# Kernel tuning notes

Measured on AMD Instinct MI355X. Metric: run time of the kernel, lower is better.

## Reference

```python
import jax, jax.numpy as jnp
import numpy as np
from jax import lax

LN_EPS = 1e-5          # F.layer_norm default eps
W_EPS = 1e-7           # eps in ste_weights
Q_EPS = 1e-5           # BitLinear.eps used in activation clamp
Q_RANGE = 128          # 2**(num_bits-1), num_bits=8
DIM_IN = 2048
DIM_OUT = 8192
N_TOKENS = 8192


def setup_inputs() -> dict:
    key = jax.random.key(0)
    k1, k2 = jax.random.split(key)
    x = jax.random.normal(k1, (N_TOKENS, DIM_IN), dtype=jnp.float32)
    # nn.Linear default init: U(-1/sqrt(fan_in), 1/sqrt(fan_in))
    bound = 1.0 / np.sqrt(DIM_IN)
    weight = jax.random.uniform(k2, (DIM_OUT, DIM_IN), dtype=jnp.float32,
                                minval=-bound, maxval=bound)
    return {"x": x, "weight": weight}


def _bitlinear(x, weight):
    # layer_norm over feature dim, no affine params
    mu = jnp.mean(x, axis=-1, keepdims=True)
    var = jnp.mean(jnp.square(x - mu), axis=-1, keepdims=True)
    normed = (x - mu) * lax.rsqrt(var + LN_EPS)

    # scalars come from .item() in torch -> detached constants
    input_gamma = lax.stop_gradient(jnp.max(jnp.abs(normed)))
    w_gamma = lax.stop_gradient(jnp.mean(jnp.abs(weight)))

    # ternarize weights with straight-through estimator
    w_bin_ng = jnp.clip(jnp.round(weight / (w_gamma + W_EPS)), -1.0, 1.0)
    w_bin = weight + lax.stop_gradient(w_bin_ng - weight)

    # quantize activations to int8 range (kept in float, as in the source)
    q_in = jnp.clip(normed * (Q_RANGE / input_gamma),
                    -Q_RANGE + Q_EPS, Q_RANGE - Q_EPS)

    out = q_in @ w_bin.T  # [N, dim_out]; bias=False since mult_bias=False
    return out * (input_gamma * w_gamma / Q_RANGE)


def reference(x, weight):
    proj = _bitlinear(x, weight)               # [N, DIM_OUT]
    h, gate = jnp.split(proj, 2, axis=-1)      # chunk(2, dim=-1)
    return h * jax.nn.silu(gate)               # mult_bias == 1.0
```

## Files before the change

kernel.cpp:

```cpp
#include <hip/hip_runtime.h>
#include <hip/hip_bf16.h>
#include <cstdint>


#define N_TOK   8192
#define DIMIN   2048
#define DIMOUT  8192
#define NOUT    4096
#define W_ELEMS 16777216.0f
#define NPART   1024

typedef _Float16 f16x8 __attribute__((ext_vector_type(8)));
typedef _Float16 f16x4 __attribute__((ext_vector_type(4)));
typedef float    f32x4 __attribute__((ext_vector_type(4)));

__global__ __launch_bounds__(256) void ln_wsum_k(
    const float* __restrict__ x, const float* __restrict__ w,
    _Float16* __restrict__ qA, float* __restrict__ wpart) {
    const int b = blockIdx.x;
    const int t = threadIdx.x;
    if (b < N_TOK) {
        __shared__ float sh[8];
        const float4* xr = (const float4*)(x + (size_t)b * DIMIN);
        float4 a = xr[2 * t];
        float4 c = xr[2 * t + 1];
        float s = (a.x + a.y) + (a.z + a.w) + ((c.x + c.y) + (c.z + c.w));
#pragma unroll
        for (int o = 32; o > 0; o >>= 1) s += __shfl_down(s, o, 64);
        if ((t & 63) == 0) sh[t >> 6] = s;
        __syncthreads();
        const float mu = (sh[0] + sh[1] + sh[2] + sh[3]) * (1.0f / DIMIN);

        float d0 = a.x - mu, d1 = a.y - mu, d2 = a.z - mu, d3 = a.w - mu;
        float d4 = c.x - mu, d5 = c.y - mu, d6 = c.z - mu, d7 = c.w - mu;
        float ss = d0*d0 + d1*d1 + d2*d2 + d3*d3 + d4*d4 + d5*d5 + d6*d6 + d7*d7;
#pragma unroll
        for (int o = 32; o > 0; o >>= 1) ss += __shfl_down(ss, o, 64);
        if ((t & 63) == 0) sh[4 + (t >> 6)] = ss;
        __syncthreads();
        const float var = (sh[4] + sh[5] + sh[6] + sh[7]) * (1.0f / DIMIN);
        const float r = rsqrtf(var + 1e-5f);
        f16x8 o;
        o[0] = (_Float16)(d0 * r); o[1] = (_Float16)(d1 * r);
        o[2] = (_Float16)(d2 * r); o[3] = (_Float16)(d3 * r);
        o[4] = (_Float16)(d4 * r); o[5] = (_Float16)(d5 * r);
        o[6] = (_Float16)(d6 * r); o[7] = (_Float16)(d7 * r);
        ((f16x8*)(qA + (size_t)b * DIMIN))[t] = o;
    } else {
        const int p = b - N_TOK;
        float acc = 0.0f;
        const float4* w4 = (const float4*)w;
        for (unsigned i = (unsigned)p * 256u + t; i < 4194304u; i += 262144u) {
            float4 v = w4[i];
            acc += (fabsf(v.x) + fabsf(v.y)) + (fabsf(v.z) + fabsf(v.w));
        }
        __shared__ float shw[4];
#pragma unroll
        for (int o = 32; o > 0; o >>= 1) acc += __shfl_down(acc, o, 64);
        if ((t & 63) == 0) shw[t >> 6] = acc;
        __syncthreads();
        if (t == 0) wpart[p] = (shw[0] + shw[1]) + (shw[2] + shw[3]);
    }
}

__global__ __launch_bounds__(256) void ternW_k(
    const float* __restrict__ w, const float* __restrict__ wpart,
    float* __restrict__ sc, _Float16* __restrict__ q) {
    const int t = threadIdx.x;
    __shared__ float sh[4];
    float4 p = ((const float4*)wpart)[t];
    float acc = (p.x + p.y) + (p.z + p.w);
#pragma unroll
    for (int o = 32; o > 0; o >>= 1) acc += __shfl_down(acc, o, 64);
    if ((t & 63) == 0) sh[t >> 6] = acc;
    __syncthreads();
    const float wg = ((sh[0] + sh[1]) + (sh[2] + sh[3])) * (1.0f / W_ELEMS);
    if (blockIdx.x == 0 && t == 0) sc[0] = wg;
    const float invw = 1.0f / (wg + 1e-7f);
    for (unsigned i = blockIdx.x * 256u + t; i < 4194304u; i += 262144u) {
        float4 v = ((const float4*)w)[i];
        f16x4 o;
        o.x = (_Float16)fminf(fmaxf(rintf(v.x * invw), -1.0f), 1.0f);
        o.y = (_Float16)fminf(fmaxf(rintf(v.y * invw), -1.0f), 1.0f);
        o.z = (_Float16)fminf(fmaxf(rintf(v.z * invw), -1.0f), 1.0f);
        o.w = (_Float16)fminf(fmaxf(rintf(v.w * invw), -1.0f), 1.0f);
        ((f16x4*)q)[i] = o;
    }
}

__device__ __forceinline__ void ld16(const _Float16* g, _Float16* l) {
    __builtin_amdgcn_global_load_lds(
        (const __attribute__((address_space(1))) unsigned int*)g,
        (__attribute__((address_space(3))) unsigned int*)l, 16, 0, 0);
}

#define STAGE(par) do {                                              \
    _Float16* dA_ = sm + ((par) << 14) + (wave << 9);                \
    _Float16* dB_ = sm + 32768 + ((par) << 14) + (wave << 9);        \
    ld16(pa,            dA_);                                        \
    ld16(pa + 131072,   dA_ + 4096);                                 \
    ld16(pa + 262144,   dA_ + 8192);                                 \
    ld16(pa + 393216,   dA_ + 12288);                                \
    ld16(pb,            dB_);                                        \
    ld16(pb + 131072,   dB_ + 4096);                                 \
    ld16(pb + 8388608,  dB_ + 8192);                                 \
    ld16(pb + 8519680,  dB_ + 12288);                                \
    pa += 64; pb += 64;                                              \
} while (0)

__global__ __launch_bounds__(512, 2) void gemm_glu_k(
    const _Float16* __restrict__ Aq, const _Float16* __restrict__ Wq,
    const float* __restrict__ sc, float* __restrict__ out) {

    __shared__ __align__(16) _Float16 sm[65536];

    const int tid  = threadIdx.x;
    const int wave = tid >> 6;
    const int lane = tid & 63;

    const int swz = ((blockIdx.x & 7) << 7) + (blockIdx.x >> 3);
    const int m0 = (swz >> 5) << 8;
    const int n0 = (swz & 31) << 7;

    const int rs = (wave << 3) + (lane >> 3);
    const int kc = (((lane & 7) ^ ((lane >> 3) & 7)) << 3);
    const _Float16* pa = Aq + (size_t)(m0 + rs) * DIMIN + kc;
    const _Float16* pb = Wq + (size_t)(n0 + rs) * DIMIN + kc;

    const int fr   = lane & 15;
    const int quad = lane >> 4;
    const int xr   = fr & 7;
    const int wm = (wave >> 1) << 6;
    const int wn = (wave & 1) << 6;
    const int a0off = (wm + fr) * 64 + ((quad ^ xr) << 3);
    const int a1off = (wm + fr) * 64 + (((quad + 4) ^ xr) << 3);
    const int b0off = (wn + fr) * 64 + ((quad ^ xr) << 3);
    const int b1off = (wn + fr) * 64 + (((quad + 4) ^ xr) << 3);

    const float s = sc[0];

    f32x4 z = {0.0f, 0.0f, 0.0f, 0.0f};
    f32x4 acc_h[4][4], acc_g[4][4];
#pragma unroll
    for (int i = 0; i < 4; ++i)
#pragma unroll
        for (int j = 0; j < 4; ++j) { acc_h[i][j] = z; acc_g[i][j] = z; }

    STAGE(0);
    asm volatile("s_waitcnt vmcnt(2)" ::: "memory");
    __builtin_amdgcn_s_barrier();

    f16x8 a[4], b[4];
#pragma unroll 2
    for (int t = 0; t < 32; ++t) {
        const _Float16* Ac = sm + ((t & 1) << 14);
        const _Float16* Bc = sm + 32768 + ((t & 1) << 14);
        const bool more = (t < 31);

#pragma unroll
        for (int i = 0; i < 4; ++i) {
            a[i] = *(const f16x8*)(Ac + a0off + (i << 10));
            b[i] = *(const f16x8*)(Bc + b0off + (i << 10));
        }
        if (more) STAGE((t + 1) & 1);
        __builtin_amdgcn_s_barrier();
        asm volatile("s_waitcnt lgkmcnt(0)" ::: "memory");
        __builtin_amdgcn_s_setprio(1);
#pragma unroll
        for (int mi = 0; mi < 4; ++mi)
#pragma unroll
            for (int ni = 0; ni < 4; ++ni)
                acc_h[mi][ni] = __builtin_amdgcn_mfma_f32_16x16x32_f16(
                    a[mi], b[ni], acc_h[mi][ni], 0, 0, 0);
        __builtin_amdgcn_s_setprio(0);
        if (more) asm volatile("s_waitcnt vmcnt(8)" ::: "memory");
        else      asm volatile("s_waitcnt vmcnt(0)" ::: "memory");
        __builtin_amdgcn_s_barrier();

#pragma unroll
        for (int i = 0; i < 4; ++i)
            b[i] = *(const f16x8*)(Bc + 8192 + b0off + (i << 10));
        __builtin_amdgcn_s_barrier();
        asm volatile("s_waitcnt lgkmcnt(0)" ::: "memory");
        __builtin_amdgcn_s_setprio(1);
#pragma unroll
        for (int mi = 0; mi < 4; ++mi)
#pragma unroll
            for (int ni = 0; ni < 4; ++ni)
                acc_g[mi][ni] = __builtin_amdgcn_mfma_f32_16x16x32_f16(
                    a[mi], b[ni], acc_g[mi][ni], 0, 0, 0);
        __builtin_amdgcn_s_setprio(0);
        __builtin_amdgcn_s_barrier();

#pragma unroll
        for (int i = 0; i < 4; ++i) {
            a[i] = *(const f16x8*)(Ac + a1off + (i << 10));
            b[i] = *(const f16x8*)(Bc + b1off + (i << 10));
        }
        __builtin_amdgcn_s_barrier();
        asm volatile("s_waitcnt lgkmcnt(0)" ::: "memory");
        __builtin_amdgcn_s_setprio(1);
#pragma unroll
        for (int mi = 0; mi < 4; ++mi)
#pragma unroll
            for (int ni = 0; ni < 4; ++ni)
                acc_h[mi][ni] = __builtin_amdgcn_mfma_f32_16x16x32_f16(
                    a[mi], b[ni], acc_h[mi][ni], 0, 0, 0);
        __builtin_amdgcn_s_setprio(0);
        __builtin_amdgcn_s_barrier();

#pragma unroll
        for (int i = 0; i < 4; ++i)
            b[i] = *(const f16x8*)(Bc + 8192 + b1off + (i << 10));
        __builtin_amdgcn_s_barrier();
        asm volatile("s_waitcnt lgkmcnt(0)" ::: "memory");
        __builtin_amdgcn_s_setprio(1);
#pragma unroll
        for (int mi = 0; mi < 4; ++mi)
#pragma unroll
            for (int ni = 0; ni < 4; ++ni)
                acc_g[mi][ni] = __builtin_amdgcn_mfma_f32_16x16x32_f16(
                    a[mi], b[ni], acc_g[mi][ni], 0, 0, 0);
        __builtin_amdgcn_s_setprio(0);
        if (more) asm volatile("s_waitcnt vmcnt(2)" ::: "memory");
        __builtin_amdgcn_s_barrier();
    }

    const int er = quad << 2;
#pragma unroll
    for (int mi = 0; mi < 4; ++mi)
#pragma unroll
        for (int ni = 0; ni < 4; ++ni)
#pragma unroll
            for (int r = 0; r < 4; ++r) {
                const int m = m0 + wm + (mi << 4) + er + r;
                const int n = n0 + wn + (ni << 4) + fr;
                const float h = acc_h[mi][ni][r] * s;
                const float g = acc_g[mi][ni][r] * s;
                out[(size_t)m * NOUT + n] = h * g / (1.0f + __expf(-g));
            }
}

extern "C" void kernel_launch(void* const* d_in, const int* in_sizes, int n_in,
                              void* d_out, int out_size, void* d_ws, size_t ws_size,
                              hipStream_t stream) {
    const float* x = (const float*)d_in[0];
    const float* w = (const float*)d_in[1];
    float* out = (float*)d_out;

    char* ws = (char*)d_ws;
    float* sc    = (float*)ws;
    float* wpart = (float*)(ws + 4096);
    _Float16* qA = (_Float16*)(ws + 16384);
    _Float16* wB = (_Float16*)(ws + 16384 + 33554432);

    ln_wsum_k<<<N_TOK + NPART, 256, 0, stream>>>(x, w, qA, wpart);
    ternW_k<<<NPART, 256, 0, stream>>>(w, wpart, sc, wB);

    gemm_glu_k<<<dim3(1024), dim3(512), 0, stream>>>(qA, wB, sc, out);
}
```

Before: 471.3 us.

## Interleave next-tile global-to-LDS loads across MFMA phases and peel last iteration

Instead of issuing all eight global-to-LDS loads for the next K tile at the start of each iteration, the loads are split into pairs spread across the four MFMA phases. The final iteration is peeled so the loop body has no 'more' conditionals. The intent is to smooth memory issue pressure and overlap loads with compute more evenly. The cost is tighter vmcnt accounting, since a missed wait could read stale LDS data, and the loop is no longer unrolled by two.

Result: faster. 450.5 us (-4.4%).

```diff
diff --git a/kernel.cpp b/kernel.cpp
--- a/kernel.cpp
+++ b/kernel.cpp
@@ -94,19 +94,28 @@
         (__attribute__((address_space(3))) unsigned int*)l, 16, 0, 0);
 }
 
-#define STAGE(par) do {                                              \
-    _Float16* dA_ = sm + ((par) << 14) + (wave << 9);                \
-    _Float16* dB_ = sm + 32768 + ((par) << 14) + (wave << 9);        \
-    ld16(pa,            dA_);                                        \
-    ld16(pa + 131072,   dA_ + 4096);                                 \
-    ld16(pa + 262144,   dA_ + 8192);                                 \
-    ld16(pa + 393216,   dA_ + 12288);                                \
-    ld16(pb,            dB_);                                        \
-    ld16(pb + 131072,   dB_ + 4096);                                 \
-    ld16(pb + 8388608,  dB_ + 8192);                                 \
-    ld16(pb + 8519680,  dB_ + 12288);                                \
-    pa += 64; pb += 64;                                              \
-} while (0)
+
+#define BAR    __builtin_amdgcn_s_barrier()
+#define LGKM0  asm volatile("s_waitcnt lgkmcnt(0)" ::: "memory")
+#define VMC(n) asm volatile("s_waitcnt vmcnt(" #n ")" ::: "memory")
+#define PRIO1  __builtin_amdgcn_s_setprio(1)
+#define PRIO0  __builtin_amdgcn_s_setprio(0)
+
+#define MFMA16(ACC)                                                       \
+    _Pragma("unroll") for (int mi = 0; mi < 4; ++mi)                      \
+    _Pragma("unroll") for (int ni = 0; ni < 4; ++ni)                      \
+        ACC[mi][ni] = __builtin_amdgcn_mfma_f32_16x16x32_f16(             \
+            a[mi], b[ni], ACC[mi][ni], 0, 0, 0);
+
+#define DS_AB(AOFF, BOFF_)                                                \
+    _Pragma("unroll") for (int i = 0; i < 4; ++i) {                       \
+        a[i] = *(const f16x8*)(Ac + (AOFF) + (i << 10));                  \
+        b[i] = *(const f16x8*)(Bc + (BOFF_) + (i << 10));                 \
+    }
+
+#define DS_B(BOFF_)                                                       \
+    _Pragma("unroll") for (int i = 0; i < 4; ++i)                         \
+        b[i] = *(const f16x8*)(Bc + (BOFF_) + (i << 10));
 
 __global__ __launch_bounds__(512, 2) void gemm_glu_k(
     const _Float16* __restrict__ Aq, const _Float16* __restrict__ Wq,
@@ -146,84 +155,85 @@
 #pragma unroll
         for (int j = 0; j < 4; ++j) { acc_h[i][j] = z; acc_g[i][j] = z; }
 
-    STAGE(0);
-    asm volatile("s_waitcnt vmcnt(2)" ::: "memory");
-    __builtin_amdgcn_s_barrier();
+    {
+        _Float16* dA = sm + (wave << 9);
+        _Float16* dB = dA + 32768;
+        ld16(pb,           dB);
+        ld16(pb + 131072,  dB + 4096);
+        ld16(pa,           dA);
+        ld16(pa + 131072,  dA + 4096);
+        ld16(pa + 262144,  dA + 8192);
+        ld16(pa + 393216,  dA + 12288);
+        ld16(pb + 8388608, dB + 8192);
+        ld16(pb + 8519680, dB + 12288);
+        pa += 64; pb += 64;
+    }
+    VMC(2);
+    BAR;
 
     f16x8 a[4], b[4];
-#pragma unroll 2
-    for (int t = 0; t < 32; ++t) {
+    for (int t = 0; t < 31; ++t) {
         const _Float16* Ac = sm + ((t & 1) << 14);
-        const _Float16* Bc = sm + 32768 + ((t & 1) << 14);
-        const bool more = (t < 31);
-
-#pragma unroll
-        for (int i = 0; i < 4; ++i) {
-            a[i] = *(const f16x8*)(Ac + a0off + (i << 10));
-            b[i] = *(const f16x8*)(Bc + b0off + (i << 10));
-        }
-        if (more) STAGE((t + 1) & 1);
-        __builtin_amdgcn_s_barrier();
-        asm volatile("s_waitcnt lgkmcnt(0)" ::: "memory");
-        __builtin_amdgcn_s_setprio(1);
-#pragma unroll
-        for (int mi = 0; mi < 4; ++mi)
-#pragma unroll
-            for (int ni = 0; ni < 4; ++ni)
-                acc_h[mi][ni] = __builtin_amdgcn_mfma_f32_16x16x32_f16(
-                    a[mi], b[ni], acc_h[mi][ni], 0, 0, 0);
-        __builtin_amdgcn_s_setprio(0);
-        if (more) asm volatile("s_waitcnt vmcnt(8)" ::: "memory");
-        else      asm volatile("s_waitcnt vmcnt(0)" ::: "memory");
-        __builtin_amdgcn_s_barrier();
-
-#pragma unroll
-        for (int i = 0; i < 4; ++i)
-            b[i] = *(const f16x8*)(Bc + 8192 + b0off + (i << 10));
-        __builtin_amdgcn_s_barrier();
-        asm volatile("s_waitcnt lgkmcnt(0)" ::: "memory");
-        __builtin_amdgcn_s_setprio(1);
-#pragma unroll
-        for (int mi = 0; mi < 4; ++mi)
-#pragma unroll
-            for (int ni = 0; ni < 4; ++ni)
-                acc_g[mi][ni] = __builtin_amdgcn_mfma_f32_16x16x32_f16(
-                    a[mi], b[ni], acc_g[mi][ni], 0, 0, 0);
-        __builtin_amdgcn_s_setprio(0);
-        __builtin_amdgcn_s_barrier();
-
-#pragma unroll
-        for (int i = 0; i < 4; ++i) {
-            a[i] = *(const f16x8*)(Ac + a1off + (i << 10));
-            b[i] = *(const f16x8*)(Bc + b1off + (i << 10));
-        }
-        __builtin_amdgcn_s_barrier();
-        asm volatile("s_waitcnt lgkmcnt(0)" ::: "memory");
-        __builtin_amdgcn_s_setprio(1);
-#pragma unroll
-        for (int mi = 0; mi < 4; ++mi)
-#pragma unroll
-            for (int ni = 0; ni < 4; ++ni)
-                acc_h[mi][ni] = __builtin_amdgcn_mfma_f32_16x16x32_f16(
-                    a[mi], b[ni], acc_h[mi][ni], 0, 0, 0);
-        __builtin_amdgcn_s_setprio(0);
-        __builtin_amdgcn_s_barrier();
-
-#pragma unroll
-        for (int i = 0; i < 4; ++i)
-            b[i] = *(const f16x8*)(Bc + 8192 + b1off + (i << 10));
-        __builtin_amdgcn_s_barrier();
-        asm volatile("s_waitcnt lgkmcnt(0)" ::: "memory");
-        __builtin_amdgcn_s_setprio(1);
-#pragma unroll
-        for (int mi = 0; mi < 4; ++mi)
-#pragma unroll
-            for (int ni = 0; ni < 4; ++ni)
-                acc_g[mi][ni] = __builtin_amdgcn_mfma_f32_16x16x32_f16(
-                    a[mi], b[ni], acc_g[mi][ni], 0, 0, 0);
-        __builtin_amdgcn_s_setprio(0);
-        if (more) asm volatile("s_waitcnt vmcnt(2)" ::: "memory");
-        __builtin_amdgcn_s_barrier();
+        const _Float16* Bc = Ac + 32768;
+        _Float16* dA = sm + (((t + 1) & 1) << 14) + (wave << 9);
+        _Float16* dB = dA + 32768;
+
+        DS_AB(a0off, b0off);
+        ld16(pb,          dB);
+        ld16(pb + 131072, dB + 4096);
+        BAR; LGKM0;
+        PRIO1; MFMA16(acc_h); PRIO0;
+        VMC(2);
+        BAR;
+
+        DS_B(8192 + b0off);
+        ld16(pa,          dA);
+        ld16(pa + 131072, dA + 4096);
+        BAR; LGKM0;
+        PRIO1; MFMA16(acc_g); PRIO0;
+        BAR;
+
+        DS_AB(a1off, b1off);
+        ld16(pa + 262144, dA + 8192);
+        ld16(pa + 393216, dA + 12288);
+        BAR; LGKM0;
+        PRIO1; MFMA16(acc_h); PRIO0;
+        BAR;
+
+        DS_B(8192 + b1off);
+        ld16(pb + 8388608, dB + 8192);
+        ld16(pb + 8519680, dB + 12288);
+        BAR; LGKM0;
+        PRIO1; MFMA16(acc_g); PRIO0;
+        VMC(2);
+        BAR;
+
+        pa += 64; pb += 64;
+    }
+
+    {
+        const _Float16* Ac = sm + 16384;
+        const _Float16* Bc = Ac + 32768;
+
+        DS_AB(a0off, b0off);
+        BAR; LGKM0;
+        PRIO1; MFMA16(acc_h); PRIO0;
+        VMC(0);
+        BAR;
+
+        DS_B(8192 + b0off);
+        BAR; LGKM0;
+        PRIO1; MFMA16(acc_g); PRIO0;
+        BAR;
+
+        DS_AB(a1off, b1off);
+        BAR; LGKM0;
+        PRIO1; MFMA16(acc_h); PRIO0;
+        BAR;
+
+        DS_B(8192 + b1off);
+        BAR; LGKM0;
+        PRIO1; MFMA16(acc_g); PRIO0;
     }
 
     const int er = quad << 2;
```
